# Kernel optimization log

Hardware: AMD Instinct MI355X
Metric: run time of the kernel (lower is better)

Reference implementation:

```python
import jax, jax.numpy as jnp
import numpy as np

N_QUBITS = 10
U3_LAYERS = 2
ENT_LAYERS = 2
EDGES = [[(q, (q + 1) % N_QUBITS) for q in range(N_QUBITS)] for _ in range(ENT_LAYERS)]
FIXED_W = [np.zeros(N_QUBITS, dtype=np.float32) for _ in range(ENT_LAYERS)]
C64 = jnp.complex64


def _rz(a):
    a = a.astype(C64)
    em, ep = jnp.exp(-0.5j * a), jnp.exp(0.5j * a)
    z = jnp.zeros((), C64)
    return jnp.stack([jnp.stack([em, z]), jnp.stack([z, ep])])


def _ry(t):
    c = jnp.cos(t / 2).astype(C64)
    s = jnp.sin(t / 2).astype(C64)
    return jnp.stack([jnp.stack([c, -s]), jnp.stack([s, c])])


def _rot(phi, theta, omega):
    # PennyLane Rot = RZ(omega) @ RY(theta) @ RZ(phi)
    return _rz(omega) @ _ry(theta) @ _rz(phi)


def _apply_1q(state, U, q):
    # state: (B,) + (2,)*n ; apply 2x2 U on qubit axis 1+q
    s = jnp.moveaxis(state, 1 + q, -1)
    s = s @ U.T
    return jnp.moveaxis(s, -1, 1 + q)


def _apply_cry(state, theta, u, v):
    U = _ry(theta)
    s = jnp.moveaxis(state, (1 + u, 1 + v), (-2, -1))  # (..., ctrl, tgt)
    c0 = s[..., 0, :]
    c1 = s[..., 1, :] @ U.T
    s = jnp.stack([c0, c1], axis=-2)
    return jnp.moveaxis(s, (-2, -1), (1 + u, 1 + v))


def _circuit(inputs, weights):
    B = inputs.shape[0]
    n = N_QUBITS
    # invert=True -> angles = pi * clamp(x, 0, 1)
    ang = jnp.pi * jnp.clip(inputs, 0.0, 1.0)
    # AngleEmbedding RY on |0...0> gives a product state
    c = jnp.cos(ang / 2).astype(C64)
    s = jnp.sin(ang / 2).astype(C64)
    st = jnp.ones((B, 1), C64)
    for q in range(n):
        amp = jnp.stack([c[:, q], s[:, q]], axis=-1)  # (B, 2)
        st = (st[:, :, None] * amp[:, None, :]).reshape(B, -1)
    st = st.reshape((B,) + (2,) * n)  # axis 1+q == wire q

    w_idx = 0
    for L in range(max(U3_LAYERS, ENT_LAYERS)):
        if L < U3_LAYERS:
            for q in range(n):
                U = _rot(weights[w_idx], weights[w_idx + 1], weights[w_idx + 2])
                w_idx += 3
                st = _apply_1q(st, U, q)
        if L < ENT_LAYERS:
            fw = FIXED_W[L]
            for i, (u, v) in enumerate(EDGES[L]):
                th = weights[w_idx] + fw[i]
                w_idx += 1
                st = _apply_cry(st, th, u, v)

    probs = (st.real ** 2 + st.imag ** 2)  # (B,) + (2,)*n
    outs = []
    for q in range(n):
        axes = tuple(a for a in range(1, n + 1) if a != 1 + q)
        m = jnp.sum(probs, axis=axes)  # (B, 2)
        outs.append(m[:, 0] - m[:, 1])
    return jnp.stack(outs, axis=-1)  # (B, n)


def setup_inputs() -> dict:
    key = jax.random.key(0)
    k1, k2 = jax.random.split(key)
    inputs = jax.random.uniform(k1, (8192, N_QUBITS), dtype=jnp.float32)
    weights = 0.1 * jax.random.normal(k2, (80,), dtype=jnp.float32)
    return {"inputs": inputs, "weights": weights}


def reference(inputs, weights):
    return _circuit(inputs, weights)
```

## Files before the change

kernel.cpp:

```cpp
#include <hip/hip_runtime.h>
#include <math.h>

#define NQ 10
typedef float v2f __attribute__((ext_vector_type(2)));

#if defined(__has_builtin)
#if __has_builtin(__builtin_amdgcn_permlane16_swap) && __has_builtin(__builtin_amdgcn_permlane32_swap)
#define HAVE_PL 1
#endif
#endif

template<int CTRL>
__device__ __forceinline__ float dppf(float x) {
    return __int_as_float(__builtin_amdgcn_update_dpp(
        __float_as_int(x), __float_as_int(x), CTRL, 0xF, 0xF, true));
}
template<int OFS>
__device__ __forceinline__ float swzf(float x) {
    return __int_as_float(__builtin_amdgcn_ds_swizzle(__float_as_int(x), OFS));
}
__device__ __forceinline__ float bperm(int idx, float x) {
    return __int_as_float(__builtin_amdgcn_ds_bpermute(idx, __float_as_int(x)));
}

template<int P>
__device__ __forceinline__ float partner1(float x) {
    if constexpr (P == 0) return dppf<0xB1>(x);
    else if constexpr (P == 1) return dppf<0x4E>(x);
    else if constexpr (P == 2) return swzf<0x101F>(x);
    else return dppf<0x128>(x);
}
template<int P>
__device__ __forceinline__ v2f partner2(v2f v) {
    v2f r; r.x = partner1<P>(v.x); r.y = partner1<P>(v.y); return r;
}

struct FPair { float v0, v1; };
template<int P>
__device__ __forceinline__ FPair blkswap1(float x, int lane) {
    FPair o;
#ifdef HAVE_PL
    if constexpr (P == 4) {
        auto r = __builtin_amdgcn_permlane16_swap(__float_as_uint(x), __float_as_uint(x), false, false);
        o.v0 = __uint_as_float(r[0]);
        o.v1 = __uint_as_float(r[1]);
    } else {
        auto r = __builtin_amdgcn_permlane32_swap(__float_as_uint(x), __float_as_uint(x), false, false);
        o.v0 = __uint_as_float(r[0]);
        o.v1 = __uint_as_float(r[1]);
    }
#else
    const float p = (P == 4) ? swzf<0x401F>(x) : bperm((lane ^ 32) << 2, x);
    const bool hi = (lane >> P) & 1;
    o.v0 = hi ? p : x;
    o.v1 = hi ? x : p;
#endif
    return o;
}
struct VPair { v2f V0, V1; };
template<int P>
__device__ __forceinline__ VPair blkswap2(v2f x, int lane) {
    const FPair a = blkswap1<P>(x.x, lane);
    const FPair b = blkswap1<P>(x.y, lane);
    VPair o;
    o.V0 = (v2f){a.v0, b.v0};
    o.V1 = (v2f){a.v1, b.v1};
    return o;
}
template<int P>
__device__ __forceinline__ float blkadd(float x, int lane) {
    const FPair o = blkswap1<P>(x, lane);
    return o.v0 + o.v1;
}

template<int P>
__device__ __forceinline__ void gate_blk_full(v2f (&Sr)[8], v2f (&Si)[8], int lane,
                                              float er, float ei, float fr, float fi) {
#pragma unroll
    for (int k = 0; k < 8; ++k) {
        const VPair R = blkswap2<P>(Sr[k], lane);
        const VPair I = blkswap2<P>(Si[k], lane);
        Sr[k] = er * R.V0 - ei * I.V0 + fr * R.V1 - fi * I.V1;
        Si[k] = er * I.V0 + ei * R.V0 + fr * I.V1 + fi * R.V1;
    }
}
template<int P>
__device__ __forceinline__ void gate_blk_real(v2f (&Sr)[8], v2f (&Si)[8], int lane,
                                              float e, float f) {
#pragma unroll
    for (int k = 0; k < 8; ++k) {
        const VPair R = blkswap2<P>(Sr[k], lane);
        const VPair I = blkswap2<P>(Si[k], lane);
        Sr[k] = e * R.V0 + f * R.V1;
        Si[k] = e * I.V0 + f * I.V1;
    }
}
template<int P>
__device__ __forceinline__ void gate_dpp_full(v2f (&Sr)[8], v2f (&Si)[8],
                                              float dr, float di, float orr, float oii) {
#pragma unroll
    for (int k = 0; k < 8; ++k) {
        const v2f mr = Sr[k], mi = Si[k];
        const v2f pr = partner2<P>(mr);
        const v2f pi = partner2<P>(mi);
        Sr[k] = dr * mr - di * mi + orr * pr - oii * pi;
        Si[k] = dr * mi + di * mr + orr * pi + oii * pr;
    }
}
template<int P>
__device__ __forceinline__ void gate_dpp_real(v2f (&Sr)[8], v2f (&Si)[8],
                                              float cl, float sgn) {
#pragma unroll
    for (int k = 0; k < 8; ++k) {
        const v2f pr = partner2<P>(Sr[k]);
        const v2f pi = partner2<P>(Si[k]);
        Sr[k] = cl * Sr[k] + sgn * pr;
        Si[k] = cl * Si[k] + sgn * pi;
    }
}
__device__ __forceinline__ void u3_pair(v2f& a0r, v2f& a0i, v2f& a1r, v2f& a1i,
                                        float u00r, float u00i, float u01r, float u01i,
                                        float u10r, float u10i, float u11r, float u11i) {
    v2f n0r = u00r * a0r - u00i * a0i + u01r * a1r - u01i * a1i;
    v2f n0i = u00r * a0i + u00i * a0r + u01r * a1i + u01i * a1r;
    v2f n1r = u10r * a0r - u10i * a0i + u11r * a1r - u11i * a1i;
    v2f n1i = u10r * a0i + u10i * a0r + u11r * a1i + u11i * a1r;
    a0r = n0r; a0i = n0i; a1r = n1r; a1i = n1i;
}
__device__ __forceinline__ void ry_pair(v2f& a0r, v2f& a0i, v2f& a1r, v2f& a1i,
                                        float c, float s) {
    v2f n0r = c * a0r - s * a1r;
    v2f n0i = c * a0i - s * a1i;
    v2f n1r = s * a0r + c * a1r;
    v2f n1i = s * a0i + c * a1i;
    a0r = n0r; a0i = n0i; a1r = n1r; a1i = n1i;
}
__device__ __forceinline__ void cmul(float& xr, float& xi, float br, float bi) {
    const float nr = xr * br - xi * bi;
    const float ni = xr * bi + xi * br;
    xr = nr; xi = ni;
}

template<int FROM>
__device__ __forceinline__ float plus_reduce(float x, int lane) {
    if constexpr (FROM <= 0) x += dppf<0xB1>(x);
    if constexpr (FROM <= 1) x += dppf<0x4E>(x);
    if constexpr (FROM <= 2) x += swzf<0x101F>(x);
    if constexpr (FROM <= 3) x += dppf<0x128>(x);
    if constexpr (FROM <= 4) x = blkadd<4>(x, lane);
    x = blkadd<5>(x, lane);
    return x;
}

__device__ __forceinline__ void makeU3(float phi, float theta, float omega, float* u) {
    const float ct = cosf(0.5f * theta), st = sinf(0.5f * theta);
    const float apo = 0.5f * (phi + omega), amo = 0.5f * (phi - omega);
    const float capo = cosf(apo), sapo = sinf(apo);
    const float camo = cosf(amo), samo = sinf(amo);
    u[0] =  capo * ct;  u[1] = -sapo * ct;
    u[2] = -camo * st;  u[3] = -samo * st;
    u[4] =  camo * st;  u[5] = -samo * st;
    u[6] =  capo * ct;  u[7] =  sapo * ct;
}

__global__ void precompute(const float* __restrict__ w, float* __restrict__ cw) {
    const int t = threadIdx.x;
    if (t < 10) {
        float u[8];
        makeU3(w[t * 3], w[t * 3 + 1], w[t * 3 + 2], u);
        float* p = cw + t * 8;
        p[0] = u[0]; p[1] = u[2];
        p[2] = u[1]; p[3] = u[3];
        p[4] = u[4]; p[5] = u[6];
        p[6] = u[5]; p[7] = u[7];
    } else if (t < 20) {
        const int q = t - 10;
        float u[8];
        makeU3(w[40 + q * 3], w[40 + q * 3 + 1], w[40 + q * 3 + 2], u);
        float* p = cw + 100 + q * 8;
        for (int i = 0; i < 8; ++i) p[i] = u[i];
    } else if (t < 29) {
        const int e = t - 20;
        const float th = 0.5f * w[30 + e];
        cw[80 + 2 * e] = cosf(th);
        cw[81 + 2 * e] = sinf(th);
    } else if (t == 29) {
        const float th = 0.5f * w[79];
        cw[98] = cosf(th);
        cw[99] = sinf(th);
    } else if (t < 40) {
        const int q = t - 30;
        float u[8];
        makeU3(w[40 + q * 3], w[40 + q * 3 + 1], w[40 + q * 3 + 2], u);
        float* p = cw + 180 + q * 8;
        if (q == 0) {
            const float th = 0.5f * w[39];
            const float ct = cosf(th), st = sinf(th);
            p[0] = u[0] * ct + u[2] * st;  p[1] = u[1] * ct + u[3] * st;
            p[2] = u[2] * ct - u[0] * st;  p[3] = u[3] * ct - u[1] * st;
            p[4] = u[4] * ct + u[6] * st;  p[5] = u[5] * ct + u[7] * st;
            p[6] = u[6] * ct - u[4] * st;  p[7] = u[7] * ct - u[5] * st;
        } else {
            const float th = 0.5f * w[70 + (q - 1)];
            const float ct = cosf(th), st = sinf(th);
            p[0] = ct * u[0] - st * u[4];  p[1] = ct * u[1] - st * u[5];
            p[2] = ct * u[2] - st * u[6];  p[3] = ct * u[3] - st * u[7];
            p[4] = st * u[0] + ct * u[4];  p[5] = st * u[1] + ct * u[5];
            p[6] = st * u[2] + ct * u[6];  p[7] = st * u[3] + ct * u[7];
        }
    }
}

#define LOADM(P, base) \
    const float P##00r = cf[(base) + 0], P##00i = cf[(base) + 1], \
                P##01r = cf[(base) + 2], P##01i = cf[(base) + 3], \
                P##10r = cf[(base) + 4], P##10i = cf[(base) + 5], \
                P##11r = cf[(base) + 6], P##11i = cf[(base) + 7];

__global__ __launch_bounds__(256) void qsim(const float* __restrict__ in,
                                            const float* __restrict__ cf,
                                            float* __restrict__ out, int B) {
    __shared__ float tsh[4 * 40];
    const int lane = threadIdx.x & 63;
    const int wave = threadIdx.x >> 6;
    int b = blockIdx.x * 4 + wave;
    b = __builtin_amdgcn_readfirstlane(b);
    if (b >= B) return;

    if (lane < 40) {
        const int q = lane >> 2;
        float x = in[b * NQ + q];
        x = fminf(fmaxf(x, 0.0f), 1.0f);
        const float a = 0.5f * 3.14159265358979323846f * x;
        const float ca = __cosf(a), sa = __sinf(a);
        const float M0 = cf[lane * 2], M1 = cf[lane * 2 + 1];
        tsh[wave * 40 + lane] = M0 * ca + M1 * sa;
    }
    const int base = wave * 40;

    float wr, wi;
    {
        const int bit = lane & 1;
        const float2 v = *(const float2*)&tsh[base + 9 * 4 + (bit << 1)];
        wr = v.x; wi = v.y;
    }
#pragma unroll
    for (int j = 1; j < 6; ++j) {
        const int bit = (lane >> j) & 1;
        const float2 v = *(const float2*)&tsh[base + (9 - j) * 4 + (bit << 1)];
        cmul(wr, wi, v.x, v.y);
    }
    const float4 T0 = *(const float4*)&tsh[base + 0];
    const float4 T1 = *(const float4*)&tsh[base + 4];
    const float4 T2 = *(const float4*)&tsh[base + 8];
    const float4 T3 = *(const float4*)&tsh[base + 12];

    float vr[4], vi[4];
    { float r = T1.x, i2 = T1.y; vr[0] = r * T2.x - i2 * T2.y; vi[0] = r * T2.y + i2 * T2.x;
                                  vr[1] = r * T2.z - i2 * T2.w; vi[1] = r * T2.w + i2 * T2.z; }
    { float r = T1.z, i2 = T1.w; vr[2] = r * T2.x - i2 * T2.y; vi[2] = r * T2.y + i2 * T2.x;
                                  vr[3] = r * T2.z - i2 * T2.w; vi[3] = r * T2.w + i2 * T2.z; }
    v2f Sr[8], Si[8];
    const v2f T0r = {T0.x, T0.z};
    const v2f T0i = {T0.y, T0.w};
#pragma unroll
    for (int k = 0; k < 8; ++k) {
        const int hv = k >> 1;
        const float t3r = (k & 1) ? T3.z : T3.x;
        const float t3i = (k & 1) ? T3.w : T3.y;
        float kr = vr[hv] * t3r - vi[hv] * t3i;
        float ki = vr[hv] * t3i + vi[hv] * t3r;
        cmul(kr, ki, wr, wi);
        Sr[k] = kr * T0r - ki * T0i;
        Si[k] = kr * T0i + ki * T0r;
    }

    {
        const float c = cf[80], s = cf[81];
        const v2f cv = {1.0f, c};
        const v2f sv = {0.0f, s};
#pragma unroll
        for (int k0 = 0; k0 < 4; ++k0) {
            const int k1 = k0 | 4;
            v2f n0r = cv * Sr[k0] - sv * Sr[k1];
            v2f n0i = cv * Si[k0] - sv * Si[k1];
            v2f n1r = sv * Sr[k0] + cv * Sr[k1];
            v2f n1i = sv * Si[k0] + cv * Si[k1];
            Sr[k0] = n0r; Si[k0] = n0i; Sr[k1] = n1r; Si[k1] = n1i;
        }
    }
    {
        const float c = cf[82], s = cf[83];
        ry_pair(Sr[4], Si[4], Sr[6], Si[6], c, s);
        ry_pair(Sr[5], Si[5], Sr[7], Si[7], c, s);
    }
    {
        const float c = cf[84], s = cf[85];
        ry_pair(Sr[2], Si[2], Sr[3], Si[3], c, s);
        ry_pair(Sr[6], Si[6], Sr[7], Si[7], c, s);
    }
    {
        const float c = cf[86], s = cf[87];
        const bool hi = (lane >> 5) & 1;
        const float e = hi ? s : c;
        const float f = hi ? c : -s;
#pragma unroll
        for (int k = 1; k < 8; k += 2) {
            const VPair R = blkswap2<5>(Sr[k], lane);
            const VPair I = blkswap2<5>(Si[k], lane);
            Sr[k] = e * R.V0 + f * R.V1;
            Si[k] = e * I.V0 + f * I.V1;
        }
    }
    {
        const float c = cf[88], s = cf[89];
        const bool ctrl = (lane >> 5) & 1;
        const bool hi = (lane >> 4) & 1;
        const float e = ctrl ? (hi ? s : c) : (hi ? 0.0f : 1.0f);
        const float f = ctrl ? (hi ? c : -s) : (hi ? 1.0f : 0.0f);
        gate_blk_real<4>(Sr, Si, lane, e, f);
    }
    {
        const float c = cf[90], s = cf[91];
        const bool ctrl = (lane >> 4) & 1;
        const float cl = ctrl ? c : 1.0f;
        const float sl = ctrl ? s : 0.0f;
        const float sgn = ((lane >> 3) & 1) ? sl : -sl;
        gate_dpp_real<3>(Sr, Si, cl, sgn);
    }
    {
        const float c = cf[92], s = cf[93];
        const bool ctrl = (lane >> 3) & 1;
        const float cl = ctrl ? c : 1.0f;
        const float sl = ctrl ? s : 0.0f;
        const float sgn = ((lane >> 2) & 1) ? sl : -sl;
        gate_dpp_real<2>(Sr, Si, cl, sgn);
    }
    {
        const float c = cf[94], s = cf[95];
        const bool ctrl = (lane >> 2) & 1;
        const float cl = ctrl ? c : 1.0f;
        const float sl = ctrl ? s : 0.0f;
        const float sgn = ((lane >> 1) & 1) ? sl : -sl;
        gate_dpp_real<1>(Sr, Si, cl, sgn);
    }
    {
        const float c = cf[96], s = cf[97];
        const bool ctrl = (lane >> 1) & 1;
        const float cl = ctrl ? c : 1.0f;
        const float sl = ctrl ? s : 0.0f;
        const float sgn = (lane & 1) ? sl : -sl;
        gate_dpp_real<0>(Sr, Si, cl, sgn);
    }

    {
        LOADM(A, 100); LOADM(Bm, 180);
        const bool ctrl = lane & 1;
        const float M00r = ctrl ? Bm00r : A00r, M00i = ctrl ? Bm00i : A00i;
        const float M01r = ctrl ? Bm01r : A01r, M01i = ctrl ? Bm01i : A01i;
        const float M10r = ctrl ? Bm10r : A10r, M10i = ctrl ? Bm10i : A10i;
        const float M11r = ctrl ? Bm11r : A11r, M11i = ctrl ? Bm11i : A11i;
        const v2f Dr = {M00r, M11r}, Di = {M00i, M11i};
        const v2f Or = {M01r, M10r}, Oi = {M01i, M10i};
#pragma unroll
        for (int k = 0; k < 8; ++k) {
            const v2f Ar = Sr[k], Ai = Si[k];
            const v2f Br = Ar.yx, Bi = Ai.yx;
            Sr[k] = Dr * Ar - Di * Ai + Or * Br - Oi * Bi;
            Si[k] = Dr * Ai + Di * Ar + Or * Bi + Oi * Br;
        }
    }
    {
        LOADM(A, 108); LOADM(Bm, 188);
        const v2f u00r = {A00r, Bm00r}, u00i = {A00i, Bm00i};
        const v2f u01r = {A01r, Bm01r}, u01i = {A01i, Bm01i};
        const v2f u10r = {A10r, Bm10r}, u10i = {A10i, Bm10i};
        const v2f u11r = {A11r, Bm11r}, u11i = {A11i, Bm11i};
#pragma unroll
        for (int k0 = 0; k0 < 4; ++k0) {
            const int k1 = k0 | 4;
            v2f n0r = u00r * Sr[k0] - u00i * Si[k0] + u01r * Sr[k1] - u01i * Si[k1];
            v2f n0i = u00r * Si[k0] + u00i * Sr[k0] + u01r * Si[k1] + u01i * Sr[k1];
            v2f n1r = u10r * Sr[k0] - u10i * Si[k0] + u11r * Sr[k1] - u11i * Si[k1];
            v2f n1i = u10r * Si[k0] + u10i * Sr[k0] + u11r * Si[k1] + u11i * Sr[k1];
            Sr[k0] = n0r; Si[k0] = n0i; Sr[k1] = n1r; Si[k1] = n1i;
        }
    }
    {
        LOADM(A, 116); LOADM(Bm, 196);
        u3_pair(Sr[0], Si[0], Sr[2], Si[2], A00r, A00i, A01r, A01i, A10r, A10i, A11r, A11i);
        u3_pair(Sr[1], Si[1], Sr[3], Si[3], A00r, A00i, A01r, A01i, A10r, A10i, A11r, A11i);
        u3_pair(Sr[4], Si[4], Sr[6], Si[6], Bm00r, Bm00i, Bm01r, Bm01i, Bm10r, Bm10i, Bm11r, Bm11i);
        u3_pair(Sr[5], Si[5], Sr[7], Si[7], Bm00r, Bm00i, Bm01r, Bm01i, Bm10r, Bm10i, Bm11r, Bm11i);
    }
    {
        LOADM(A, 124); LOADM(Bm, 204);
        u3_pair(Sr[0], Si[0], Sr[1], Si[1], A00r, A00i, A01r, A01i, A10r, A10i, A11r, A11i);
        u3_pair(Sr[4], Si[4], Sr[5], Si[5], A00r, A00i, A01r, A01i, A10r, A10i, A11r, A11i);
        u3_pair(Sr[2], Si[2], Sr[3], Si[3], Bm00r, Bm00i, Bm01r, Bm01i, Bm10r, Bm10i, Bm11r, Bm11i);
        u3_pair(Sr[6], Si[6], Sr[7], Si[7], Bm00r, Bm00i, Bm01r, Bm01i, Bm10r, Bm10i, Bm11r, Bm11i);
    }
    {
        LOADM(A, 132); LOADM(Bm, 212);
        const bool hi = (lane >> 5) & 1;
        const float eAr = hi ? A10r : A00r, eAi = hi ? A10i : A00i;
        const float fAr = hi ? A11r : A01r, fAi = hi ? A11i : A01i;
        const float eBr = hi ? Bm10r : Bm00r, eBi = hi ? Bm10i : Bm00i;
        const float fBr = hi ? Bm11r : Bm01r, fBi = hi ? Bm11i : Bm01i;
#pragma unroll
        for (int k = 0; k < 8; ++k) {
            const float er = (k & 1) ? eBr : eAr, ei = (k & 1) ? eBi : eAi;
            const float fr = (k & 1) ? fBr : fAr, fi = (k & 1) ? fBi : fAi;
            const VPair R = blkswap2<5>(Sr[k], lane);
            const VPair I = blkswap2<5>(Si[k], lane);
            Sr[k] = er * R.V0 - ei * I.V0 + fr * R.V1 - fi * I.V1;
            Si[k] = er * I.V0 + ei * R.V0 + fr * I.V1 + fi * R.V1;
        }
    }
    {
        LOADM(A, 140); LOADM(Bm, 220);
        const bool ctrl = (lane >> 5) & 1;
        const bool hi = (lane >> 4) & 1;
        const float M00r = ctrl ? Bm00r : A00r, M00i = ctrl ? Bm00i : A00i;
        const float M01r = ctrl ? Bm01r : A01r, M01i = ctrl ? Bm01i : A01i;
        const float M10r = ctrl ? Bm10r : A10r, M10i = ctrl ? Bm10i : A10i;
        const float M11r = ctrl ? Bm11r : A11r, M11i = ctrl ? Bm11i : A11i;
        const float er = hi ? M10r : M00r, ei = hi ? M10i : M00i;
        const float fr = hi ? M11r : M01r, fi = hi ? M11i : M01i;
        gate_blk_full<4>(Sr, Si, lane, er, ei, fr, fi);
    }
    {
        LOADM(A, 148); LOADM(Bm, 228);
        const bool ctrl = (lane >> 4) & 1;
        const bool hi = (lane >> 3) & 1;
        const float M00r = ctrl ? Bm00r : A00r, M00i = ctrl ? Bm00i : A00i;
        const float M01r = ctrl ? Bm01r : A01r, M01i = ctrl ? Bm01i : A01i;
        const float M10r = ctrl ? Bm10r : A10r, M10i = ctrl ? Bm10i : A10i;
        const float M11r = ctrl ? Bm11r : A11r, M11i = ctrl ? Bm11i : A11i;
        const float dr = hi ? M11r : M00r, di = hi ? M11i : M00i;
        const float orr = hi ? M10r : M01r, oii = hi ? M10i : M01i;
        gate_dpp_full<3>(Sr, Si, dr, di, orr, oii);
    }
    {
        LOADM(A, 156); LOADM(Bm, 236);
        const bool ctrl = (lane >> 3) & 1;
        const bool hi = (lane >> 2) & 1;
        const float M00r = ctrl ? Bm00r : A00r, M00i = ctrl ? Bm00i : A00i;
        const float M01r = ctrl ? Bm01r : A01r, M01i = ctrl ? Bm01i : A01i;
        const float M10r = ctrl ? Bm10r : A10r, M10i = ctrl ? Bm10i : A10i;
        const float M11r = ctrl ? Bm11r : A11r, M11i = ctrl ? Bm11i : A11i;
        const float dr = hi ? M11r : M00r, di = hi ? M11i : M00i;
        const float orr = hi ? M10r : M01r, oii = hi ? M10i : M01i;
        gate_dpp_full<2>(Sr, Si, dr, di, orr, oii);
    }
    {
        LOADM(A, 164); LOADM(Bm, 244);
        const bool ctrl = (lane >> 2) & 1;
        const bool hi = (lane >> 1) & 1;
        const float M00r = ctrl ? Bm00r : A00r, M00i = ctrl ? Bm00i : A00i;
        const float M01r = ctrl ? Bm01r : A01r, M01i = ctrl ? Bm01i : A01i;
        const float M10r = ctrl ? Bm10r : A10r, M10i = ctrl ? Bm10i : A10i;
        const float M11r = ctrl ? Bm11r : A11r, M11i = ctrl ? Bm11i : A11i;
        const float dr = hi ? M11r : M00r, di = hi ? M11i : M00i;
        const float orr = hi ? M10r : M01r, oii = hi ? M10i : M01i;
        gate_dpp_full<1>(Sr, Si, dr, di, orr, oii);
    }
    {
        LOADM(A, 172); LOADM(Bm, 252);
        const bool ctrl = (lane >> 1) & 1;
        const bool hi = lane & 1;
        const float M00r = ctrl ? Bm00r : A00r, M00i = ctrl ? Bm00i : A00i;
        const float M01r = ctrl ? Bm01r : A01r, M01i = ctrl ? Bm01i : A01i;
        const float M10r = ctrl ? Bm10r : A10r, M10i = ctrl ? Bm10i : A10i;
        const float M11r = ctrl ? Bm11r : A11r, M11i = ctrl ? Bm11i : A11i;
        const float dr = hi ? M11r : M00r, di = hi ? M11i : M00i;
        const float orr = hi ? M10r : M01r, oii = hi ? M10i : M01i;
        gate_dpp_full<0>(Sr, Si, dr, di, orr, oii);
    }
    {
        const float c = cf[98], s = cf[99];
        const bool ctrl = lane & 1;
        const float cl = ctrl ? c : 1.0f;
        const float sl = ctrl ? s : 0.0f;
        const v2f C2 = {cl, cl};
        const v2f S2 = {-sl, sl};
#pragma unroll
        for (int k = 0; k < 8; ++k) {
            const v2f Ar = Sr[k], Ai = Si[k];
            Sr[k] = C2 * Ar + S2 * Ar.yx;
            Si[k] = C2 * Ai + S2 * Ai.yx;
        }
    }

    v2f P[8];
    float ptot = 0.0f, z0p = 0.0f, z1p = 0.0f, z2p = 0.0f, z3p = 0.0f;
#pragma unroll
    for (int k = 0; k < 8; ++k) {
        P[k] = Sr[k] * Sr[k] + Si[k] * Si[k];
        const float sk = P[k].x + P[k].y;
        ptot += sk;
        z0p += P[k].x - P[k].y;
        z1p += ((k >> 2) & 1) ? -sk : sk;
        z2p += ((k >> 1) & 1) ? -sk : sk;
        z3p += (k & 1) ? -sk : sk;
    }
    float d0, d1, d2, d3, d4, d5;
    {
        float a = ptot, p;
        p = dppf<0xB1>(a);   d0 = a - p; a += p;
        p = dppf<0x4E>(a);   d1 = a - p; a += p;
        p = swzf<0x101F>(a); d2 = a - p; a += p;
        p = dppf<0x128>(a);  d3 = a - p; a += p;
        { const FPair o = blkswap1<4>(a, lane); d4 = o.v0 - o.v1; a = o.v0 + o.v1; }
        { const FPair o = blkswap1<5>(a, lane); d5 = o.v0 - o.v1; }
    }
    float z[NQ];
    z[0] = plus_reduce<0>(z0p, lane);
    z[1] = plus_reduce<0>(z1p, lane);
    z[2] = plus_reduce<0>(z2p, lane);
    z[3] = plus_reduce<0>(z3p, lane);
    z[4] = d5;
    z[5] = plus_reduce<5>(d4, lane);
    z[6] = plus_reduce<4>(d3, lane);
    z[7] = plus_reduce<3>(d2, lane);
    z[8] = plus_reduce<2>(d1, lane);
    z[9] = plus_reduce<1>(d0, lane);

    if (lane == 0) {
#pragma unroll
        for (int q = 0; q < NQ; ++q) out[b * NQ + q] = z[q];
    }
}

extern "C" void kernel_launch(void* const* d_in, const int* in_sizes, int n_in,
                              void* d_out, int out_size, void* d_ws, size_t ws_size,
                              hipStream_t stream) {
    const float* inputs  = (const float*)d_in[0];
    const float* weights = (const float*)d_in[1];
    float* out = (float*)d_out;
    float* cw  = (float*)d_ws;
    const int B = in_sizes[0] / NQ;

    precompute<<<1, 64, 0, stream>>>(weights, cw);
    qsim<<<(B + 3) / 4, 256, 0, stream>>>(inputs, cw, out, B);
}
```

Before: 87.91 us.

## Fuse gate-matrix precompute into qsim kernel via per-wave LDS table

Removes the separate single-block precompute launch; each wave now rebuilds the U3, CRY and fused gate coefficients from the raw weights with fast intrinsics and keeps them in its own LDS slice. All coefficient reads change from scalar global loads to vectorised LDS loads. This drops one kernel launch and its serial dependency, at the cost of redundant trig work in every wave, more LDS per block, and lower-accuracy __cosf/__sinf in place of cosf/sinf. There is no barrier after the LDS writes, which relies on wave-local execution order.

```diff
diff --git a/kernel.cpp b/kernel.cpp
--- a/kernel.cpp
+++ b/kernel.cpp
@@ -152,80 +152,72 @@
     return x;
 }
 
-__device__ __forceinline__ void makeU3(float phi, float theta, float omega, float* u) {
-    const float ct = cosf(0.5f * theta), st = sinf(0.5f * theta);
-    const float apo = 0.5f * (phi + omega), amo = 0.5f * (phi - omega);
-    const float capo = cosf(apo), sapo = sinf(apo);
-    const float camo = cosf(amo), samo = sinf(amo);
-    u[0] =  capo * ct;  u[1] = -sapo * ct;
-    u[2] = -camo * st;  u[3] = -samo * st;
-    u[4] =  camo * st;  u[5] = -samo * st;
-    u[6] =  capo * ct;  u[7] =  sapo * ct;
-}
-
-__global__ void precompute(const float* __restrict__ w, float* __restrict__ cw) {
-    const int t = threadIdx.x;
-    if (t < 10) {
-        float u[8];
-        makeU3(w[t * 3], w[t * 3 + 1], w[t * 3 + 2], u);
-        float* p = cw + t * 8;
-        p[0] = u[0]; p[1] = u[2];
-        p[2] = u[1]; p[3] = u[3];
-        p[4] = u[4]; p[5] = u[6];
-        p[6] = u[5]; p[7] = u[7];
-    } else if (t < 20) {
-        const int q = t - 10;
-        float u[8];
-        makeU3(w[40 + q * 3], w[40 + q * 3 + 1], w[40 + q * 3 + 2], u);
-        float* p = cw + 100 + q * 8;
-        for (int i = 0; i < 8; ++i) p[i] = u[i];
-    } else if (t < 29) {
-        const int e = t - 20;
-        const float th = 0.5f * w[30 + e];
-        cw[80 + 2 * e] = cosf(th);
-        cw[81 + 2 * e] = sinf(th);
-    } else if (t == 29) {
-        const float th = 0.5f * w[79];
-        cw[98] = cosf(th);
-        cw[99] = sinf(th);
-    } else if (t < 40) {
-        const int q = t - 30;
-        float u[8];
-        makeU3(w[40 + q * 3], w[40 + q * 3 + 1], w[40 + q * 3 + 2], u);
-        float* p = cw + 180 + q * 8;
-        if (q == 0) {
-            const float th = 0.5f * w[39];
-            const float ct = cosf(th), st = sinf(th);
-            p[0] = u[0] * ct + u[2] * st;  p[1] = u[1] * ct + u[3] * st;
-            p[2] = u[2] * ct - u[0] * st;  p[3] = u[3] * ct - u[1] * st;
-            p[4] = u[4] * ct + u[6] * st;  p[5] = u[5] * ct + u[7] * st;
-            p[6] = u[6] * ct - u[4] * st;  p[7] = u[7] * ct - u[5] * st;
-        } else {
-            const float th = 0.5f * w[70 + (q - 1)];
-            const float ct = cosf(th), st = sinf(th);
-            p[0] = ct * u[0] - st * u[4];  p[1] = ct * u[1] - st * u[5];
-            p[2] = ct * u[2] - st * u[6];  p[3] = ct * u[3] - st * u[7];
-            p[4] = st * u[0] + ct * u[4];  p[5] = st * u[1] + ct * u[5];
-            p[6] = st * u[2] + ct * u[6];  p[7] = st * u[3] + ct * u[7];
-        }
-    }
-}
-
 #define LOADM(P, base) \
-    const float P##00r = cf[(base) + 0], P##00i = cf[(base) + 1], \
-                P##01r = cf[(base) + 2], P##01i = cf[(base) + 3], \
-                P##10r = cf[(base) + 4], P##10i = cf[(base) + 5], \
-                P##11r = cf[(base) + 6], P##11i = cf[(base) + 7];
+    const float4 P##va = *(const float4*)&cs[(base)]; \
+    const float4 P##vb = *(const float4*)&cs[(base) + 4]; \
+    const float P##00r = P##va.x, P##00i = P##va.y, P##01r = P##va.z, P##01i = P##va.w, \
+                P##10r = P##vb.x, P##10i = P##vb.y, P##11r = P##vb.z, P##11i = P##vb.w;
+
 
 __global__ __launch_bounds__(256) void qsim(const float* __restrict__ in,
-                                            const float* __restrict__ cf,
+                                            const float* __restrict__ w,
                                             float* __restrict__ out, int B) {
-    __shared__ float tsh[4 * 40];
+    __shared__ __attribute__((aligned(16))) float csh[4 * 272];
+    __shared__ __attribute__((aligned(16))) float tsh[4 * 40];
     const int lane = threadIdx.x & 63;
     const int wave = threadIdx.x >> 6;
     int b = blockIdx.x * 4 + wave;
     b = __builtin_amdgcn_readfirstlane(b);
     if (b >= B) return;
+    float* cs = csh + wave * 272;
+
+    {
+        const int q = (lane < 20) ? (lane % 10) : ((lane >= 40 && lane < 50) ? lane - 40 : 0);
+        const int wb = (lane < 10) ? 3 * lane : 40 + 3 * q;
+        const float phi = w[wb], theta = w[wb + 1], omega = w[wb + 2];
+        float u0, u1, u2, u3, u4, u5, u6, u7;
+        {
+            const float ct = __cosf(0.5f * theta), st = __sinf(0.5f * theta);
+            const float apo = 0.5f * (phi + omega), amo = 0.5f * (phi - omega);
+            const float capo = __cosf(apo), sapo = __sinf(apo);
+            const float camo = __cosf(amo), samo = __sinf(amo);
+            u0 =  capo * ct;  u1 = -sapo * ct;
+            u2 = -camo * st;  u3 = -samo * st;
+            u4 =  camo * st;  u5 = -samo * st;
+            u6 =  capo * ct;  u7 =  sapo * ct;
+        }
+        const int cidx = (lane >= 20 && lane < 29) ? 30 + (lane - 20)
+                       : (lane == 29) ? 79
+                       : (lane == 40) ? 39
+                       : 70 + (q - 1) + (q == 0 ? 1 : 0);
+        const float th = 0.5f * w[cidx];
+        const float c2 = __cosf(th), s2 = __sinf(th);
+        if (lane >= 40 && lane < 50) {
+            const bool r = (lane == 40);
+            const float p0 = r ? (u0 * c2 + u2 * s2) : (c2 * u0 - s2 * u4);
+            const float p1 = r ? (u1 * c2 + u3 * s2) : (c2 * u1 - s2 * u5);
+            const float p2 = r ? (u2 * c2 - u0 * s2) : (c2 * u2 - s2 * u6);
+            const float p3 = r ? (u3 * c2 - u1 * s2) : (c2 * u3 - s2 * u7);
+            const float p4 = r ? (u4 * c2 + u6 * s2) : (s2 * u0 + c2 * u4);
+            const float p5 = r ? (u5 * c2 + u7 * s2) : (s2 * u1 + c2 * u5);
+            const float p6 = r ? (u6 * c2 - u4 * s2) : (s2 * u2 + c2 * u6);
+            const float p7 = r ? (u7 * c2 - u5 * s2) : (s2 * u3 + c2 * u7);
+            u0 = p0; u1 = p1; u2 = p2; u3 = p3; u4 = p4; u5 = p5; u6 = p6; u7 = p7;
+        }
+        if (lane < 10) {
+            *(float4*)&cs[lane * 8]     = (float4){u0, u2, u1, u3};
+            *(float4*)&cs[lane * 8 + 4] = (float4){u4, u6, u5, u7};
+        } else if (lane < 20) {
+            *(float4*)&cs[100 + (lane - 10) * 8]     = (float4){u0, u1, u2, u3};
+            *(float4*)&cs[100 + (lane - 10) * 8 + 4] = (float4){u4, u5, u6, u7};
+        } else if (lane < 30) {
+            const int off = (lane < 29) ? 80 + 2 * (lane - 20) : 98;
+            *(float2*)&cs[off] = (float2){c2, s2};
+        } else if (lane >= 40 && lane < 50) {
+            *(float4*)&cs[180 + q * 8]     = (float4){u0, u1, u2, u3};
+            *(float4*)&cs[180 + q * 8 + 4] = (float4){u4, u5, u6, u7};
+        }
+    }
 
     if (lane < 40) {
         const int q = lane >> 2;
@@ -233,7 +225,7 @@
         x = fminf(fmaxf(x, 0.0f), 1.0f);
         const float a = 0.5f * 3.14159265358979323846f * x;
         const float ca = __cosf(a), sa = __sinf(a);
-        const float M0 = cf[lane * 2], M1 = cf[lane * 2 + 1];
+        const float M0 = cs[lane * 2], M1 = cs[lane * 2 + 1];
         tsh[wave * 40 + lane] = M0 * ca + M1 * sa;
     }
     const int base = wave * 40;
@@ -276,9 +268,9 @@
     }
 
     {
-        const float c = cf[80], s = cf[81];
-        const v2f cv = {1.0f, c};
-        const v2f sv = {0.0f, s};
+        const float2 C = *(const float2*)&cs[80];
+        const v2f cv = {1.0f, C.x};
+        const v2f sv = {0.0f, C.y};
 #pragma unroll
         for (int k0 = 0; k0 < 4; ++k0) {
             const int k1 = k0 | 4;
@@ -290,20 +282,20 @@
         }
     }
     {
-        const float c = cf[82], s = cf[83];
-        ry_pair(Sr[4], Si[4], Sr[6], Si[6], c, s);
-        ry_pair(Sr[5], Si[5], Sr[7], Si[7], c, s);
-    }
-    {
-        const float c = cf[84], s = cf[85];
-        ry_pair(Sr[2], Si[2], Sr[3], Si[3], c, s);
-        ry_pair(Sr[6], Si[6], Sr[7], Si[7], c, s);
-    }
-    {
-        const float c = cf[86], s = cf[87];
+        const float2 C = *(const float2*)&cs[82];
+        ry_pair(Sr[4], Si[4], Sr[6], Si[6], C.x, C.y);
+        ry_pair(Sr[5], Si[5], Sr[7], Si[7], C.x, C.y);
+    }
+    {
+        const float2 C = *(const float2*)&cs[84];
+        ry_pair(Sr[2], Si[2], Sr[3], Si[3], C.x, C.y);
+        ry_pair(Sr[6], Si[6], Sr[7], Si[7], C.x, C.y);
+    }
+    {
+        const float2 C = *(const float2*)&cs[86];
         const bool hi = (lane >> 5) & 1;
-        const float e = hi ? s : c;
-        const float f = hi ? c : -s;
+        const float e = hi ? C.y : C.x;
+        const float f = hi ? C.x : -C.y;
 #pragma unroll
         for (int k = 1; k < 8; k += 2) {
             const VPair R = blkswap2<5>(Sr[k], lane);
@@ -313,42 +305,42 @@
         }
     }
     {
-        const float c = cf[88], s = cf[89];
+        const float2 C = *(const float2*)&cs[88];
         const bool ctrl = (lane >> 5) & 1;
         const bool hi = (lane >> 4) & 1;
-        const float e = ctrl ? (hi ? s : c) : (hi ? 0.0f : 1.0f);
-        const float f = ctrl ? (hi ? c : -s) : (hi ? 1.0f : 0.0f);
+        const float e = ctrl ? (hi ? C.y : C.x) : (hi ? 0.0f : 1.0f);
+        const float f = ctrl ? (hi ? C.x : -C.y) : (hi ? 1.0f : 0.0f);
         gate_blk_real<4>(Sr, Si, lane, e, f);
     }
     {
-        const float c = cf[90], s = cf[91];
+        const float2 C = *(const float2*)&cs[90];
         const bool ctrl = (lane >> 4) & 1;
-        const float cl = ctrl ? c : 1.0f;
-        const float sl = ctrl ? s : 0.0f;
+        const float cl = ctrl ? C.x : 1.0f;
+        const float sl = ctrl ? C.y : 0.0f;
         const float sgn = ((lane >> 3) & 1) ? sl : -sl;
         gate_dpp_real<3>(Sr, Si, cl, sgn);
     }
     {
-        const float c = cf[92], s = cf[93];
+        const float2 C = *(const float2*)&cs[92];
         const bool ctrl = (lane >> 3) & 1;
-        const float cl = ctrl ? c : 1.0f;
-        const float sl = ctrl ? s : 0.0f;
+        const float cl = ctrl ? C.x : 1.0f;
+        const float sl = ctrl ? C.y : 0.0f;
         const float sgn = ((lane >> 2) & 1) ? sl : -sl;
         gate_dpp_real<2>(Sr, Si, cl, sgn);
     }
     {
-        const float c = cf[94], s = cf[95];
+        const float2 C = *(const float2*)&cs[94];
         const bool ctrl = (lane >> 2) & 1;
-        const float cl = ctrl ? c : 1.0f;
-        const float sl = ctrl ? s : 0.0f;
+        const float cl = ctrl ? C.x : 1.0f;
+        const float sl = ctrl ? C.y : 0.0f;
         const float sgn = ((lane >> 1) & 1) ? sl : -sl;
         gate_dpp_real<1>(Sr, Si, cl, sgn);
     }
     {
-        const float c = cf[96], s = cf[97];
+        const float2 C = *(const float2*)&cs[96];
         const bool ctrl = (lane >> 1) & 1;
-        const float cl = ctrl ? c : 1.0f;
-        const float sl = ctrl ? s : 0.0f;
+        const float cl = ctrl ? C.x : 1.0f;
+        const float sl = ctrl ? C.y : 0.0f;
         const float sgn = (lane & 1) ? sl : -sl;
         gate_dpp_real<0>(Sr, Si, cl, sgn);
     }
@@ -478,10 +470,10 @@
         gate_dpp_full<0>(Sr, Si, dr, di, orr, oii);
     }
     {
-        const float c = cf[98], s = cf[99];
+        const float2 C = *(const float2*)&cs[98];
         const bool ctrl = lane & 1;
-        const float cl = ctrl ? c : 1.0f;
-        const float sl = ctrl ? s : 0.0f;
+        const float cl = ctrl ? C.x : 1.0f;
+        const float sl = ctrl ? C.y : 0.0f;
         const v2f C2 = {cl, cl};
         const v2f S2 = {-sl, sl};
 #pragma unroll
@@ -538,9 +530,7 @@
     const float* inputs  = (const float*)d_in[0];
     const float* weights = (const float*)d_in[1];
     float* out = (float*)d_out;
-    float* cw  = (float*)d_ws;
     const int B = in_sizes[0] / NQ;
 
-    precompute<<<1, 64, 0, stream>>>(weights, cw);
-    qsim<<<(B + 3) / 4, 256, 0, stream>>>(inputs, cw, out, B);
-}
+    qsim<<<(B + 3) / 4, 256, 0, stream>>>(inputs, weights, out, B);
+}
```

Result: faster. 82.35 us (-6.3%).
